# Kernel tuning notes

Measured on AMD Instinct MI355X. Metric: run time of the kernel, lower is better.

## Reference

```python
import jax, jax.numpy as jnp
import numpy as np

N_HEAD = 16
D_MODEL = 1024


def setup_inputs() -> dict:
    key = jax.random.key(0)
    ks = jax.random.split(key, 12)
    B, S, D = 2, 2048, D_MODEL
    s = 0.02
    return {
        "q": jax.random.normal(ks[0], (B, S, D), jnp.float32),
        "k": jax.random.normal(ks[1], (B, S, D), jnp.float32),
        "v": jax.random.normal(ks[2], (B, S, 2 * D), jnp.float32),
        "Wq": jax.random.normal(ks[3], (D, D), jnp.float32) * s,
        "bq": jnp.zeros((D,), jnp.float32),
        "Wk": jax.random.normal(ks[4], (D, D), jnp.float32) * s,
        "bk": jnp.zeros((D,), jnp.float32),
        "Wv": jax.random.normal(ks[5], (2 * D, D), jnp.float32) * s,
        "bv": jnp.zeros((D,), jnp.float32),
        "Wfc": jax.random.normal(ks[6], (D, 2 * D), jnp.float32) * s,
        "bfc": jnp.zeros((2 * D,), jnp.float32),
        "padding_mask": jnp.ones((B, S), jnp.int32),
    }


def reference(q, k, v, Wq, bq, Wk, bk, Wv, bv, Wfc, bfc, padding_mask):
    B, S, D = q.shape
    H = N_HEAD
    dh = D // H
    scale = jnp.float32(np.sqrt(dh))
    # projections, split heads -> [B, H, S, dh]
    qh = (q @ Wq + bq).reshape(B, S, H, dh).transpose(0, 2, 1, 3)
    kh = (k @ Wk + bk).reshape(B, S, H, dh).transpose(0, 2, 1, 3)
    vh = (v @ Wv + bv).reshape(B, S, H, dh).transpose(0, 2, 1, 3)
    # scores [B, H, S, S]
    attn = jnp.einsum("bhqd,bhkd->bhqk", qh, kh) / scale
    pad = (padding_mask == 0)[:, None, None, :]  # [B,1,1,S]
    attn = jnp.where(pad, -jnp.inf, attn)
    attn = jax.nn.softmax(attn, axis=-1)
    # dropout p=0 in eval -> identity
    out = jnp.einsum("bhqk,bhkd->bhqd", attn, vh)
    out = out.transpose(0, 2, 1, 3).reshape(B, S, D)
    out = out @ Wfc + bfc  # [B, S, 2D]
    attn_avg = attn.sum(axis=1) / H  # [B, S, S]
    return out, attn_avg
```

## Files before the change

kernel.cpp:

```cpp
#include <hip/hip_runtime.h>
#include <math.h>

#define BATCH   2
#define SLEN    2048
#define DMODEL  1024
#define NHEAD   16
#define DHEAD   64
#define DOUT    2048
#define MROWS   (BATCH * SLEN)
#define NSPLIT  2
#define KSPAN   (SLEN / NSPLIT)

typedef short bf16x8 __attribute__((ext_vector_type(8)));
typedef float floatx4 __attribute__((ext_vector_type(4)));

static __device__ __forceinline__ unsigned short f2bf(float f) {
  unsigned u = __float_as_uint(f);
  u += 0x7fff + ((u >> 16) & 1);
  return (unsigned short)(u >> 16);
}
static __device__ __forceinline__ float bf2f(unsigned short s) {
  return __uint_as_float(((unsigned)s) << 16);
}
static __device__ __forceinline__ floatx4 mfma16(bf16x8 a, bf16x8 b, floatx4 c) {
  return __builtin_amdgcn_mfma_f32_16x16x32_bf16(a, b, c, 0, 0, 0);
}
static __device__ __forceinline__ void gll16(const void* g, void* l) {
  __builtin_amdgcn_global_load_lds(
      (const __attribute__((address_space(1))) unsigned int*)g,
      (__attribute__((address_space(3))) unsigned int*)l, 16, 0, 0);
}

__global__ __launch_bounds__(256) void conv_all_k(
    const float* __restrict__ q, const float* __restrict__ k,
    const float* __restrict__ v, unsigned short* __restrict__ qb,
    unsigned short* __restrict__ kb, unsigned short* __restrict__ vb) {
  int i = blockIdx.x * 256 + threadIdx.x;
  const float* src;
  unsigned short* dst;
  if (i < (1 << 19)) { src = q; dst = qb; }
  else if (i < (1 << 20)) { src = k; dst = kb; i -= 1 << 19; }
  else { src = v; dst = vb; i -= 1 << 20; }
  const float4 a = ((const float4*)src)[i * 2];
  const float4 b = ((const float4*)src)[i * 2 + 1];
  ushort4 u0, u1;
  u0.x = f2bf(a.x); u0.y = f2bf(a.y); u0.z = f2bf(a.z); u0.w = f2bf(a.w);
  u1.x = f2bf(b.x); u1.y = f2bf(b.y); u1.z = f2bf(b.z); u1.w = f2bf(b.w);
  ((ushort4*)dst)[i * 2] = u0;
  ((ushort4*)dst)[i * 2 + 1] = u1;
}

__global__ __launch_bounds__(256) void wtrans_all_k(
    const float* __restrict__ Wq, const float* __restrict__ Wk,
    const float* __restrict__ Wv, const float* __restrict__ Wfc,
    unsigned short* __restrict__ WqT, unsigned short* __restrict__ WkT,
    unsigned short* __restrict__ WvT, unsigned short* __restrict__ WfcT) {
  __shared__ float T[32][33];
  int id = blockIdx.x;
  const float* W;
  unsigned short* WT;
  int K, N;
  if (id < 1024)      { W = Wq;  WT = WqT;  K = 1024; N = 1024; }
  else if (id < 2048) { W = Wk;  WT = WkT;  K = 1024; N = 1024; id -= 1024; }
  else if (id < 4096) { W = Wv;  WT = WvT;  K = 2048; N = 1024; id -= 2048; }
  else                { W = Wfc; WT = WfcT; K = 1024; N = 2048; id -= 4096; }
  const int ntn = N / 32;
  const int n0 = (id % ntn) * 32, k0 = (id / ntn) * 32;
  const int t = threadIdx.x;
  {
    const int r = t >> 3, c4 = (t & 7) * 4;
    const float4 w = *(const float4*)(W + (size_t)(k0 + r) * N + n0 + c4);
    T[r][c4 + 0] = w.x; T[r][c4 + 1] = w.y; T[r][c4 + 2] = w.z; T[r][c4 + 3] = w.w;
  }
  __syncthreads();
  {
    const int n = t >> 3, k4 = (t & 7) * 4;
    ushort4 u;
    u.x = f2bf(T[k4 + 0][n]); u.y = f2bf(T[k4 + 1][n]);
    u.z = f2bf(T[k4 + 2][n]); u.w = f2bf(T[k4 + 3][n]);
    *(ushort4*)(WT + (size_t)(n0 + n) * K + k0 + k4) = u;
  }
}

template <int MODE>
static __device__ __forceinline__ void gemm_body(
    const unsigned short* __restrict__ A, const unsigned short* __restrict__ BT,
    const float* __restrict__ bias, void* __restrict__ C, int M, int K, int N,
    int row0, int col0) {
  __shared__ unsigned short As[128 * 64];
  __shared__ unsigned short Bs[64 * 64];
  const int t = threadIdx.x;
  const int w = t >> 6, l = t & 63, quad = l >> 4, lq = l & 15;
  const int wm = (w >> 1) * 64, wn = (w & 1) * 32;

  const unsigned short* aS[4];
#pragma unroll
  for (int jj = 0; jj < 4; jj++) {
    const int m = (w * 4 + jj) * 8 + (l >> 3);
    aS[jj] = A + (size_t)(row0 + m) * K + (((l & 7) ^ (m & 7)) << 3);
  }
  const unsigned short* bS[2];
#pragma unroll
  for (int jj = 0; jj < 2; jj++) {
    const int n = (w * 2 + jj) * 8 + (l >> 3);
    bS[jj] = BT + (size_t)(col0 + n) * K + (((l & 7) ^ (n & 7)) << 3);
  }

  floatx4 acc[4][2];
#pragma unroll
  for (int i = 0; i < 4; i++)
#pragma unroll
    for (int j = 0; j < 2; j++) acc[i][j] = (floatx4){0.f, 0.f, 0.f, 0.f};

  for (int kt = 0; kt < K; kt += 64) {
#pragma unroll
    for (int jj = 0; jj < 4; jj++)
      gll16(aS[jj] + kt, As + (w * 4 + jj) * 512);
#pragma unroll
    for (int jj = 0; jj < 2; jj++)
      gll16(bS[jj] + kt, Bs + (w * 2 + jj) * 512);
    __syncthreads();

    bf16x8 af[4][2], bfr[2][2];
#pragma unroll
    for (int ti = 0; ti < 4; ti++) {
      const int m = wm + ti * 16 + lq;
#pragma unroll
      for (int h = 0; h < 2; h++)
        af[ti][h] = *(const bf16x8*)(As + m * 64 + (((h * 4 + quad) ^ (m & 7)) << 3));
    }
#pragma unroll
    for (int tj = 0; tj < 2; tj++) {
      const int n = wn + tj * 16 + lq;
#pragma unroll
      for (int h = 0; h < 2; h++)
        bfr[tj][h] = *(const bf16x8*)(Bs + n * 64 + (((h * 4 + quad) ^ (n & 7)) << 3));
    }
#pragma unroll
    for (int ti = 0; ti < 4; ti++)
#pragma unroll
      for (int tj = 0; tj < 2; tj++) {
        acc[ti][tj] = mfma16(af[ti][0], bfr[tj][0], acc[ti][tj]);
        acc[ti][tj] = mfma16(af[ti][1], bfr[tj][1], acc[ti][tj]);
      }
    __syncthreads();
  }

#pragma unroll
  for (int tj = 0; tj < 2; tj++) {
    const int col = col0 + wn + tj * 16 + lq;
    const float bv = bias[col];
    if (MODE == 2) {
#pragma unroll
      for (int ti = 0; ti < 4; ti++) {
        ushort4 u;
        u.x = f2bf(acc[ti][tj][0] + bv);
        u.y = f2bf(acc[ti][tj][1] + bv);
        u.z = f2bf(acc[ti][tj][2] + bv);
        u.w = f2bf(acc[ti][tj][3] + bv);
        *(ushort4*)((unsigned short*)C + (size_t)col * M + row0 + wm + ti * 16 +
                    quad * 4) = u;
      }
    } else {
#pragma unroll
      for (int ti = 0; ti < 4; ti++)
#pragma unroll
        for (int r = 0; r < 4; r++) {
          const int row = row0 + wm + ti * 16 + quad * 4 + r;
          const float vv = acc[ti][tj][r] + bv;
          if (MODE == 1)
            ((float*)C)[(size_t)row * N + col] = vv;
          else
            ((unsigned short*)C)[(size_t)row * N + col] = f2bf(vv);
        }
    }
  }
}

__global__ __launch_bounds__(256) void qkproj_k(
    const unsigned short* qb, const unsigned short* kb,
    const unsigned short* WqT, const unsigned short* WkT,
    const float* bq, const float* bk,
    unsigned short* Qp, unsigned short* Kp) {
  const int z = blockIdx.z;
  gemm_body<0>(z ? kb : qb, z ? WkT : WqT, z ? bk : bq, z ? Kp : Qp,
               MROWS, DMODEL, DMODEL, blockIdx.y * 128, blockIdx.x * 64);
}
__global__ __launch_bounds__(256) void vproj_k(
    const unsigned short* vb, const unsigned short* WvT, const float* bv,
    unsigned short* VT) {
  gemm_body<2>(vb, WvT, bv, VT, MROWS, 2 * DMODEL, DMODEL,
               blockIdx.y * 128, blockIdx.x * 64);
}
__global__ __launch_bounds__(256) void fc_k(
    const unsigned short* att, const unsigned short* WfcT, const float* bfc,
    float* out) {
  gemm_body<1>(att, WfcT, bfc, out, MROWS, DMODEL, DOUT,
               blockIdx.y * 128, blockIdx.x * 64);
}

__global__ __launch_bounds__(256) void flash_mfma_k(
    const unsigned short* __restrict__ Qp, const unsigned short* __restrict__ Kp,
    const unsigned short* __restrict__ VT, const int* __restrict__ mask,
    unsigned short* __restrict__ Opart, float* __restrict__ Lpart) {
  __shared__ unsigned short Ks[64 * 64];
  __shared__ unsigned short Vs[64 * 64];
  __shared__ unsigned short Ps[4][16 * 68];
  const int t = threadIdx.x;
  const int w = t >> 6, l = t & 63, quad = l >> 4, lq = l & 15;
  const int q0 = blockIdx.x * 64;
  const int h = blockIdx.y >> 1, split = blockIdx.y & 1;
  const int b = blockIdx.z;

  const unsigned short* qptr =
      Qp + (size_t)(b * SLEN + q0 + w * 16 + lq) * DMODEL + h * 64;
  const bf16x8 aq0 = *(const bf16x8*)(qptr + quad * 8);
  const bf16x8 aq1 = *(const bf16x8*)(qptr + 32 + quad * 8);

  int krow[2], kchunk[2];
#pragma unroll
  for (int jj = 0; jj < 2; jj++) {
    krow[jj] = (w * 2 + jj) * 8 + (l >> 3);
    kchunk[jj] = (l & 7) ^ (krow[jj] & 7);
  }
  const unsigned short* Kbase = Kp + (size_t)b * SLEN * DMODEL + h * 64;
  const unsigned short* Vbase = VT + (size_t)h * 64 * MROWS + b * SLEN;

  floatx4 acc_o[4];
#pragma unroll
  for (int dj = 0; dj < 4; dj++) acc_o[dj] = (floatx4){0.f, 0.f, 0.f, 0.f};
  float lsum = 0.f;
  unsigned short* PsW = &Ps[w][0];

  for (int k0 = split * KSPAN; k0 < split * KSPAN + KSPAN; k0 += 64) {
    __syncthreads();
#pragma unroll
    for (int jj = 0; jj < 2; jj++) {
      const int inst = w * 2 + jj;
      gll16(Kbase + (size_t)(k0 + krow[jj]) * DMODEL + kchunk[jj] * 8,
            Ks + inst * 512);
      gll16(Vbase + (size_t)krow[jj] * MROWS + k0 + kchunk[jj] * 8,
            Vs + inst * 512);
    }
    __syncthreads();

#pragma unroll
    for (int ti = 0; ti < 4; ti++) {
      const int kk = ti * 16 + lq;
      const bf16x8 bk0 = *(const bf16x8*)(Ks + kk * 64 + ((quad ^ (kk & 7)) << 3));
      const bf16x8 bk1 =
          *(const bf16x8*)(Ks + kk * 64 + (((4 + quad) ^ (kk & 7)) << 3));
      floatx4 z = (floatx4){0.f, 0.f, 0.f, 0.f};
      z = mfma16(bk0, aq0, z);
      z = mfma16(bk1, aq1, z);
      const int4 m4 = *(const int4*)(mask + b * SLEN + k0 + ti * 16 + quad * 4);
      const int mv[4] = {m4.x, m4.y, m4.z, m4.w};
      float e[4];
#pragma unroll
      for (int r = 0; r < 4; r++) {
        float ev = __expf(z[r] * 0.125f);
        ev = mv[r] ? ev : 0.f;
        e[r] = ev;
        lsum += ev;
      }
      ushort4 u;
      u.x = f2bf(e[0]); u.y = f2bf(e[1]); u.z = f2bf(e[2]); u.w = f2bf(e[3]);
      *(ushort4*)(PsW + lq * 68 + ti * 16 + quad * 4) = u;
    }
    __asm__ __volatile__("" ::: "memory");
    const bf16x8 ap0 = *(const bf16x8*)(PsW + lq * 68 + quad * 8);
    const bf16x8 ap1 = *(const bf16x8*)(PsW + lq * 68 + 32 + quad * 8);
#pragma unroll
    for (int dj = 0; dj < 4; dj++) {
      const int d = dj * 16 + lq;
      const bf16x8 bv0 = *(const bf16x8*)(Vs + d * 64 + ((quad ^ (d & 7)) << 3));
      const bf16x8 bv1 =
          *(const bf16x8*)(Vs + d * 64 + (((4 + quad) ^ (d & 7)) << 3));
      acc_o[dj] = mfma16(ap0, bv0, acc_o[dj]);
      acc_o[dj] = mfma16(ap1, bv1, acc_o[dj]);
    }
  }

  lsum += __shfl_xor(lsum, 16);
  lsum += __shfl_xor(lsum, 32);

  const size_t obase =
      (((size_t)split * BATCH + b) * NHEAD + h) * SLEN + q0 + w * 16;
#pragma unroll
  for (int dj = 0; dj < 4; dj++)
#pragma unroll
    for (int r = 0; r < 4; r++)
      Opart[(obase + quad * 4 + r) * DHEAD + dj * 16 + lq] = f2bf(acc_o[dj][r]);
  if (quad == 0) Lpart[obase + lq] = lsum;
}

__global__ __launch_bounds__(256) void combine_k(
    const unsigned short* __restrict__ Opart, const float* __restrict__ Lpart,
    unsigned short* __restrict__ att, float* __restrict__ lbuf) {
  const int gid = blockIdx.x * 256 + threadIdx.x;
  const int row = gid >> 3;
  const int d8 = (gid & 7) * 8;
  const float l0 = Lpart[row];
  const float l1 = Lpart[(size_t)BATCH * NHEAD * SLEN + row];
  const float lt = l0 + l1;
  const float il = (lt > 0.f) ? 1.f / lt : 0.f;
  const bf16x8 o0 = *(const bf16x8*)(Opart + (size_t)row * DHEAD + d8);
  const bf16x8 o1 = *(const bf16x8*)(Opart + (size_t)(BATCH * NHEAD * SLEN) * DHEAD +
                                     (size_t)row * DHEAD + d8);
  const int b = row >> 15, hh = (row >> 11) & 15, q = row & 2047;
  unsigned short* dst = att + (size_t)(b * SLEN + q) * DMODEL + hh * 64 + d8;
  ushort4 u0, u1;
  float vv[8];
#pragma unroll
  for (int j = 0; j < 8; j++)
    vv[j] = (bf2f((unsigned short)o0[j]) + bf2f((unsigned short)o1[j])) * il;
  u0.x = f2bf(vv[0]); u0.y = f2bf(vv[1]); u0.z = f2bf(vv[2]); u0.w = f2bf(vv[3]);
  u1.x = f2bf(vv[4]); u1.y = f2bf(vv[5]); u1.z = f2bf(vv[6]); u1.w = f2bf(vv[7]);
  ((ushort4*)dst)[0] = u0;
  ((ushort4*)dst)[1] = u1;
  if ((gid & 7) == 0) lbuf[row] = lt;
}

__global__ __launch_bounds__(256) void attn_avg_mfma_k(
    const unsigned short* __restrict__ Qp, const unsigned short* __restrict__ Kp,
    const float* __restrict__ lbuf, const int* __restrict__ mask,
    float* __restrict__ aout) {
  __shared__ unsigned short Ks[64 * 64];
  const int t = threadIdx.x;
  const int w = t >> 6, l = t & 63, quad = l >> 4, lq = l & 15;
  const int k0 = blockIdx.x * 64, q0 = blockIdx.y * 64, b = blockIdx.z;

  floatx4 acc[4];
#pragma unroll
  for (int ti = 0; ti < 4; ti++) acc[ti] = (floatx4){0.f, 0.f, 0.f, 0.f};
  int mk[4];
#pragma unroll
  for (int ti = 0; ti < 4; ti++) mk[ti] = mask[b * SLEN + k0 + ti * 16 + lq];

  int krow[2], kchunk[2];
#pragma unroll
  for (int jj = 0; jj < 2; jj++) {
    krow[jj] = (w * 2 + jj) * 8 + (l >> 3);
    kchunk[jj] = (l & 7) ^ (krow[jj] & 7);
  }
  const unsigned short* Kbase = Kp + (size_t)(b * SLEN + k0) * DMODEL;
  const unsigned short* qbase =
      Qp + (size_t)(b * SLEN + q0 + w * 16 + lq) * DMODEL;

  for (int h = 0; h < NHEAD; h++) {
    __syncthreads();
#pragma unroll
    for (int jj = 0; jj < 2; jj++)
      gll16(Kbase + (size_t)krow[jj] * DMODEL + h * 64 + kchunk[jj] * 8,
            Ks + (w * 2 + jj) * 512);
    __syncthreads();

    const bf16x8 aq0 = *(const bf16x8*)(qbase + h * 64 + quad * 8);
    const bf16x8 aq1 = *(const bf16x8*)(qbase + h * 64 + 32 + quad * 8);
    float ilr[4];
#pragma unroll
    for (int r = 0; r < 4; r++) {
      const float lv = lbuf[(b * NHEAD + h) * SLEN + q0 + w * 16 + quad * 4 + r];
      ilr[r] = (lv > 0.f) ? 1.f / lv : 0.f;
    }
#pragma unroll
    for (int ti = 0; ti < 4; ti++) {
      const int kk = ti * 16 + lq;
      const bf16x8 bk0 = *(const bf16x8*)(Ks + kk * 64 + ((quad ^ (kk & 7)) << 3));
      const bf16x8 bk1 =
          *(const bf16x8*)(Ks + kk * 64 + (((4 + quad) ^ (kk & 7)) << 3));
      floatx4 z = (floatx4){0.f, 0.f, 0.f, 0.f};
      z = mfma16(aq0, bk0, z);
      z = mfma16(aq1, bk1, z);
#pragma unroll
      for (int r = 0; r < 4; r++)
        acc[ti][r] += mk[ti] ? __expf(z[r] * 0.125f) * ilr[r] : 0.f;
    }
  }
  const float ih = 1.f / NHEAD;
#pragma unroll
  for (int ti = 0; ti < 4; ti++)
#pragma unroll
    for (int r = 0; r < 4; r++)
      aout[(size_t)(b * SLEN + q0 + w * 16 + quad * 4 + r) * SLEN + k0 +
           ti * 16 + lq] = acc[ti][r] * ih;
}

extern "C" void kernel_launch(void* const* d_in, const int* in_sizes, int n_in,
                              void* d_out, int out_size, void* d_ws, size_t ws_size,
                              hipStream_t stream) {
  const float* q   = (const float*)d_in[0];
  const float* k   = (const float*)d_in[1];
  const float* v   = (const float*)d_in[2];
  const float* Wq  = (const float*)d_in[3];
  const float* bq  = (const float*)d_in[4];
  const float* Wk  = (const float*)d_in[5];
  const float* bk  = (const float*)d_in[6];
  const float* Wv  = (const float*)d_in[7];
  const float* bv  = (const float*)d_in[8];
  const float* Wfc = (const float*)d_in[9];
  const float* bfc = (const float*)d_in[10];
  const int* mask  = (const int*)d_in[11];

  float* out      = (float*)d_out;
  float* attn_avg = out + (size_t)MROWS * DOUT;

  unsigned short* qb = (unsigned short*)d_out;
  unsigned short* kb = qb + (1u << 22);
  unsigned short* vb = kb + (1u << 22);
  unsigned short* Opart = (unsigned short*)d_out;
  float* Lpart = (float*)((char*)d_out + (size_t)NSPLIT * BATCH * NHEAD * SLEN * DHEAD * 2);

  unsigned short* wsb  = (unsigned short*)d_ws;
  unsigned short* WqT  = wsb;
  unsigned short* WkT  = wsb + (1u << 20);
  unsigned short* WvT  = wsb + (2u << 20);
  unsigned short* WfcT = wsb + (4u << 20);
  unsigned short* Qp   = wsb + (6u << 20);
  unsigned short* Kp   = Qp + (1u << 22);
  unsigned short* VT   = Kp + (1u << 22);
  unsigned short* att  = VT + (1u << 22);
  float* lbuf = (float*)(att + (1u << 22));

  conv_all_k<<<dim3(8192), dim3(256), 0, stream>>>(q, k, v, qb, kb, vb);
  wtrans_all_k<<<dim3(6144), dim3(256), 0, stream>>>(Wq, Wk, Wv, Wfc,
                                                     WqT, WkT, WvT, WfcT);
  qkproj_k<<<dim3(DMODEL / 64, MROWS / 128, 2), dim3(256), 0, stream>>>(
      qb, kb, WqT, WkT, bq, bk, Qp, Kp);
  vproj_k<<<dim3(DMODEL / 64, MROWS / 128), dim3(256), 0, stream>>>(
      vb, WvT, bv, VT);
  flash_mfma_k<<<dim3(SLEN / 64, NHEAD * NSPLIT, BATCH), dim3(256), 0, stream>>>(
      Qp, Kp, VT, mask, Opart, Lpart);
  combine_k<<<dim3(BATCH * NHEAD * SLEN * DHEAD / 8 / 256), dim3(256), 0, stream>>>(
      Opart, Lpart, att, lbuf);
  attn_avg_mfma_k<<<dim3(SLEN / 64, SLEN / 64, BATCH), dim3(256), 0, stream>>>(
      Qp, Kp, lbuf, mask, attn_avg);
  fc_k<<<dim3(DOUT / 64, MROWS / 128), dim3(256), 0, stream>>>(
      att, WfcT, bfc, out);
}
```

Before: 373.3 us.

## Merge Q/K/V projections into one launch, use packed bf16 converts and LDS mask bias

Merges the Q/K and V projection GEMMs into a single three-slice launch, which removes one kernel boundary and lets the blocks overlap. Every bf16 conversion now goes through a packed two-value convert using the gfx950 builtin when available, with wider stores. The flash and attn-average kernels precompute an additive mask bias (0 or -inf) and the inverse row sums in shared memory, which replaces per-tile global mask and lbuf loads and the select. Adds LDS use and a prologue in each block; with -inf bias, exp gives 0 for masked keys, matching the old select.

```diff
diff --git a/kernel.cpp b/kernel.cpp
--- a/kernel.cpp
+++ b/kernel.cpp
@@ -21,6 +21,15 @@
 }
 static __device__ __forceinline__ float bf2f(unsigned short s) {
   return __uint_as_float(((unsigned)s) << 16);
+}
+static __device__ __forceinline__ unsigned int pk_bf16(float a, float b) {
+#if defined(__gfx950__) && __has_builtin(__builtin_amdgcn_cvt_pk_bf16_f32)
+  typedef __bf16 bf2_t __attribute__((ext_vector_type(2)));
+  bf2_t r = __builtin_amdgcn_cvt_pk_bf16_f32(a, b);
+  return __builtin_bit_cast(unsigned int, r);
+#else
+  return ((unsigned)f2bf(b) << 16) | f2bf(a);
+#endif
 }
 static __device__ __forceinline__ floatx4 mfma16(bf16x8 a, bf16x8 b, floatx4 c) {
   return __builtin_amdgcn_mfma_f32_16x16x32_bf16(a, b, c, 0, 0, 0);
@@ -43,11 +52,12 @@
   else { src = v; dst = vb; i -= 1 << 20; }
   const float4 a = ((const float4*)src)[i * 2];
   const float4 b = ((const float4*)src)[i * 2 + 1];
-  ushort4 u0, u1;
-  u0.x = f2bf(a.x); u0.y = f2bf(a.y); u0.z = f2bf(a.z); u0.w = f2bf(a.w);
-  u1.x = f2bf(b.x); u1.y = f2bf(b.y); u1.z = f2bf(b.z); u1.w = f2bf(b.w);
-  ((ushort4*)dst)[i * 2] = u0;
-  ((ushort4*)dst)[i * 2 + 1] = u1;
+  uint4 u;
+  u.x = pk_bf16(a.x, a.y);
+  u.y = pk_bf16(a.z, a.w);
+  u.z = pk_bf16(b.x, b.y);
+  u.w = pk_bf16(b.z, b.w);
+  ((uint4*)dst)[i] = u;
 }
 
 __global__ __launch_bounds__(256) void wtrans_all_k(
@@ -75,10 +85,10 @@
   __syncthreads();
   {
     const int n = t >> 3, k4 = (t & 7) * 4;
-    ushort4 u;
-    u.x = f2bf(T[k4 + 0][n]); u.y = f2bf(T[k4 + 1][n]);
-    u.z = f2bf(T[k4 + 2][n]); u.w = f2bf(T[k4 + 3][n]);
-    *(ushort4*)(WT + (size_t)(n0 + n) * K + k0 + k4) = u;
+    uint2 u;
+    u.x = pk_bf16(T[k4 + 0][n], T[k4 + 1][n]);
+    u.y = pk_bf16(T[k4 + 2][n], T[k4 + 3][n]);
+    *(uint2*)(WT + (size_t)(n0 + n) * K + k0 + k4) = u;
   }
 }
 
@@ -153,13 +163,11 @@
     if (MODE == 2) {
 #pragma unroll
       for (int ti = 0; ti < 4; ti++) {
-        ushort4 u;
-        u.x = f2bf(acc[ti][tj][0] + bv);
-        u.y = f2bf(acc[ti][tj][1] + bv);
-        u.z = f2bf(acc[ti][tj][2] + bv);
-        u.w = f2bf(acc[ti][tj][3] + bv);
-        *(ushort4*)((unsigned short*)C + (size_t)col * M + row0 + wm + ti * 16 +
-                    quad * 4) = u;
+        uint2 u;
+        u.x = pk_bf16(acc[ti][tj][0] + bv, acc[ti][tj][1] + bv);
+        u.y = pk_bf16(acc[ti][tj][2] + bv, acc[ti][tj][3] + bv);
+        *(uint2*)((unsigned short*)C + (size_t)col * M + row0 + wm + ti * 16 +
+                  quad * 4) = u;
       }
     } else {
 #pragma unroll
@@ -177,20 +185,22 @@
   }
 }
 
-__global__ __launch_bounds__(256) void qkproj_k(
-    const unsigned short* qb, const unsigned short* kb,
+__global__ __launch_bounds__(256) void proj_k(
+    const unsigned short* qb, const unsigned short* kb, const unsigned short* vb,
     const unsigned short* WqT, const unsigned short* WkT,
-    const float* bq, const float* bk,
-    unsigned short* Qp, unsigned short* Kp) {
+    const unsigned short* WvT, const float* bq, const float* bk,
+    const float* bv, unsigned short* Qp, unsigned short* Kp,
+    unsigned short* VT) {
   const int z = blockIdx.z;
-  gemm_body<0>(z ? kb : qb, z ? WkT : WqT, z ? bk : bq, z ? Kp : Qp,
-               MROWS, DMODEL, DMODEL, blockIdx.y * 128, blockIdx.x * 64);
-}
-__global__ __launch_bounds__(256) void vproj_k(
-    const unsigned short* vb, const unsigned short* WvT, const float* bv,
-    unsigned short* VT) {
-  gemm_body<2>(vb, WvT, bv, VT, MROWS, 2 * DMODEL, DMODEL,
-               blockIdx.y * 128, blockIdx.x * 64);
+  if (z == 2)
+    gemm_body<2>(vb, WvT, bv, VT, MROWS, 2 * DMODEL, DMODEL,
+                 blockIdx.y * 128, blockIdx.x * 64);
+  else if (z == 1)
+    gemm_body<0>(kb, WkT, bk, Kp, MROWS, DMODEL, DMODEL,
+                 blockIdx.y * 128, blockIdx.x * 64);
+  else
+    gemm_body<0>(qb, WqT, bq, Qp, MROWS, DMODEL, DMODEL,
+                 blockIdx.y * 128, blockIdx.x * 64);
 }
 __global__ __launch_bounds__(256) void fc_k(
     const unsigned short* att, const unsigned short* WfcT, const float* bfc,
@@ -206,12 +216,16 @@
   __shared__ unsigned short Ks[64 * 64];
   __shared__ unsigned short Vs[64 * 64];
   __shared__ unsigned short Ps[4][16 * 68];
+  __shared__ float biasL[KSPAN];
   const int t = threadIdx.x;
   const int w = t >> 6, l = t & 63, quad = l >> 4, lq = l & 15;
   const int q0 = blockIdx.x * 64;
   const int h = blockIdx.y >> 1, split = blockIdx.y & 1;
   const int b = blockIdx.z;
 
+  for (int i = t; i < KSPAN; i += 256)
+    biasL[i] = mask[b * SLEN + split * KSPAN + i] ? 0.f : -INFINITY;
+
   const unsigned short* qptr =
       Qp + (size_t)(b * SLEN + q0 + w * 16 + lq) * DMODEL + h * 64;
   const bf16x8 aq0 = *(const bf16x8*)(qptr + quad * 8);
@@ -232,7 +246,8 @@
   float lsum = 0.f;
   unsigned short* PsW = &Ps[w][0];
 
-  for (int k0 = split * KSPAN; k0 < split * KSPAN + KSPAN; k0 += 64) {
+  for (int k0s = 0; k0s < KSPAN; k0s += 64) {
+    const int k0 = split * KSPAN + k0s;
     __syncthreads();
 #pragma unroll
     for (int jj = 0; jj < 2; jj++) {
@@ -253,19 +268,16 @@
       floatx4 z = (floatx4){0.f, 0.f, 0.f, 0.f};
       z = mfma16(bk0, aq0, z);
       z = mfma16(bk1, aq1, z);
-      const int4 m4 = *(const int4*)(mask + b * SLEN + k0 + ti * 16 + quad * 4);
-      const int mv[4] = {m4.x, m4.y, m4.z, m4.w};
-      float e[4];
-#pragma unroll
-      for (int r = 0; r < 4; r++) {
-        float ev = __expf(z[r] * 0.125f);
-        ev = mv[r] ? ev : 0.f;
-        e[r] = ev;
-        lsum += ev;
-      }
-      ushort4 u;
-      u.x = f2bf(e[0]); u.y = f2bf(e[1]); u.z = f2bf(e[2]); u.w = f2bf(e[3]);
-      *(ushort4*)(PsW + lq * 68 + ti * 16 + quad * 4) = u;
+      const float4 bb = *(const float4*)&biasL[k0s + ti * 16 + quad * 4];
+      const float e0 = __expf(fmaf(z[0], 0.125f, bb.x));
+      const float e1 = __expf(fmaf(z[1], 0.125f, bb.y));
+      const float e2 = __expf(fmaf(z[2], 0.125f, bb.z));
+      const float e3 = __expf(fmaf(z[3], 0.125f, bb.w));
+      lsum += (e0 + e1) + (e2 + e3);
+      uint2 pk;
+      pk.x = pk_bf16(e0, e1);
+      pk.y = pk_bf16(e2, e3);
+      *(uint2*)(PsW + lq * 68 + ti * 16 + quad * 4) = pk;
     }
     __asm__ __volatile__("" ::: "memory");
     const bf16x8 ap0 = *(const bf16x8*)(PsW + lq * 68 + quad * 8);
@@ -309,15 +321,16 @@
                                      (size_t)row * DHEAD + d8);
   const int b = row >> 15, hh = (row >> 11) & 15, q = row & 2047;
   unsigned short* dst = att + (size_t)(b * SLEN + q) * DMODEL + hh * 64 + d8;
-  ushort4 u0, u1;
   float vv[8];
 #pragma unroll
   for (int j = 0; j < 8; j++)
     vv[j] = (bf2f((unsigned short)o0[j]) + bf2f((unsigned short)o1[j])) * il;
-  u0.x = f2bf(vv[0]); u0.y = f2bf(vv[1]); u0.z = f2bf(vv[2]); u0.w = f2bf(vv[3]);
-  u1.x = f2bf(vv[4]); u1.y = f2bf(vv[5]); u1.z = f2bf(vv[6]); u1.w = f2bf(vv[7]);
-  ((ushort4*)dst)[0] = u0;
-  ((ushort4*)dst)[1] = u1;
+  uint4 u;
+  u.x = pk_bf16(vv[0], vv[1]);
+  u.y = pk_bf16(vv[2], vv[3]);
+  u.z = pk_bf16(vv[4], vv[5]);
+  u.w = pk_bf16(vv[6], vv[7]);
+  *(uint4*)dst = u;
   if ((gid & 7) == 0) lbuf[row] = lt;
 }
 
@@ -326,16 +339,23 @@
     const float* __restrict__ lbuf, const int* __restrict__ mask,
     float* __restrict__ aout) {
   __shared__ unsigned short Ks[64 * 64];
+  __shared__ float ilL[NHEAD * 64];
   const int t = threadIdx.x;
   const int w = t >> 6, l = t & 63, quad = l >> 4, lq = l & 15;
   const int k0 = blockIdx.x * 64, q0 = blockIdx.y * 64, b = blockIdx.z;
 
+  for (int i = t; i < NHEAD * 64; i += 256) {
+    const float lv = lbuf[(b * NHEAD + (i >> 6)) * SLEN + q0 + (i & 63)];
+    ilL[i] = (lv > 0.f) ? 1.f / lv : 0.f;
+  }
+  float bb[4];
+#pragma unroll
+  for (int ti = 0; ti < 4; ti++)
+    bb[ti] = mask[b * SLEN + k0 + ti * 16 + lq] ? 0.f : -INFINITY;
+
   floatx4 acc[4];
 #pragma unroll
   for (int ti = 0; ti < 4; ti++) acc[ti] = (floatx4){0.f, 0.f, 0.f, 0.f};
-  int mk[4];
-#pragma unroll
-  for (int ti = 0; ti < 4; ti++) mk[ti] = mask[b * SLEN + k0 + ti * 16 + lq];
 
   int krow[2], kchunk[2];
 #pragma unroll
@@ -357,12 +377,8 @@
 
     const bf16x8 aq0 = *(const bf16x8*)(qbase + h * 64 + quad * 8);
     const bf16x8 aq1 = *(const bf16x8*)(qbase + h * 64 + 32 + quad * 8);
-    float ilr[4];
-#pragma unroll
-    for (int r = 0; r < 4; r++) {
-      const float lv = lbuf[(b * NHEAD + h) * SLEN + q0 + w * 16 + quad * 4 + r];
-      ilr[r] = (lv > 0.f) ? 1.f / lv : 0.f;
-    }
+    const float4 il4 = *(const float4*)&ilL[h * 64 + w * 16 + quad * 4];
+    const float ila[4] = {il4.x, il4.y, il4.z, il4.w};
 #pragma unroll
     for (int ti = 0; ti < 4; ti++) {
       const int kk = ti * 16 + lq;
@@ -374,7 +390,7 @@
       z = mfma16(aq1, bk1, z);
 #pragma unroll
       for (int r = 0; r < 4; r++)
-        acc[ti][r] += mk[ti] ? __expf(z[r] * 0.125f) * ilr[r] : 0.f;
+        acc[ti][r] = fmaf(__expf(fmaf(z[r], 0.125f, bb[ti])), ila[r], acc[ti][r]);
     }
   }
   const float ih = 1.f / NHEAD;
@@ -425,10 +441,8 @@
   conv_all_k<<<dim3(8192), dim3(256), 0, stream>>>(q, k, v, qb, kb, vb);
   wtrans_all_k<<<dim3(6144), dim3(256), 0, stream>>>(Wq, Wk, Wv, Wfc,
                                                      WqT, WkT, WvT, WfcT);
-  qkproj_k<<<dim3(DMODEL / 64, MROWS / 128, 2), dim3(256), 0, stream>>>(
-      qb, kb, WqT, WkT, bq, bk, Qp, Kp);
-  vproj_k<<<dim3(DMODEL / 64, MROWS / 128), dim3(256), 0, stream>>>(
-      vb, WvT, bv, VT);
+  proj_k<<<dim3(DMODEL / 64, MROWS / 128, 3), dim3(256), 0, stream>>>(
+      qb, kb, vb, WqT, WkT, WvT, bq, bk, bv, Qp, Kp, VT);
   flash_mfma_k<<<dim3(SLEN / 64, NHEAD * NSPLIT, BATCH), dim3(256), 0, stream>>>(
       Qp, Kp, VT, mask, Opart, Lpart);
   combine_k<<<dim3(BATCH * NHEAD * SLEN * DHEAD / 8 / 256), dim3(256), 0, stream>>>(
```

Result: no change. 367.2 us (-1.6%).
